# Performance work log

Measured on AMD Instinct MI355X. Metric: run time of the kernel, lower is better.

The kernel has to match this reference:

```python
import jax, jax.numpy as jnp
import numpy as np

N = 100000      # nodes
E = 1600000     # edges
F_IN = 128      # num_node_features
C = 8           # num_classes
EPS = 1e-5


def _lin_init(key, fi, fo):
    k1, k2 = jax.random.split(key)
    s = 1.0 / np.sqrt(fi)
    W = jax.random.uniform(k1, (fi, fo), jnp.float32, -s, s)
    b = jax.random.uniform(k2, (fo,), jnp.float32, -s, s)
    return W, b


def _bn_init(key, f):
    k1, k2, k3, k4 = jax.random.split(key, 4)
    gamma = 1.0 + 0.1 * jax.random.normal(k1, (f,), jnp.float32)
    beta = 0.1 * jax.random.normal(k2, (f,), jnp.float32)
    mean = 0.1 * jax.random.normal(k3, (f,), jnp.float32)
    var = jax.random.uniform(k4, (f,), jnp.float32, 0.5, 1.5)
    return gamma, beta, mean, var


def setup_inputs() -> dict:
    key = jax.random.key(0)
    ks = jax.random.split(key, 10)
    p = {}
    p["x"] = jax.random.normal(ks[0], (N, F_IN), jnp.float32)
    p["edge_index"] = jax.random.randint(ks[1], (2, E), 0, N, jnp.int32)
    p["W1"], p["b1"] = _lin_init(ks[2], F_IN, 64)
    p["g1"], p["be1"], p["m1"], p["v1"] = _bn_init(ks[3], 64)
    p["W2"], p["b2"] = _lin_init(ks[4], 64, 32)
    p["g2"], p["be2"], p["m2"], p["v2"] = _bn_init(ks[5], 32)
    p["W3"], p["b3"] = _lin_init(ks[6], 32, 16)
    p["g3"], p["be3"], p["m3"], p["v3"] = _bn_init(ks[7], 16)
    p["fcW"], p["fcb"] = _lin_init(ks[8], 16, C)
    return p


def _gcn_conv(h, W, b, src, dst, dinv):
    # GCNConv: transform, then symmetric-normalized aggregation with self-loops.
    hw = h @ W                                   # [N, Fout]
    coef = (dinv[src] * dinv[dst])[:, None]      # [E, 1]
    agg = jax.ops.segment_sum(hw[src] * coef, dst, num_segments=N)
    agg = agg + hw * (dinv * dinv)[:, None]      # self-loop contribution
    return agg + b


def _bn(h, g, be, m, v):
    # eval-mode BatchNorm1d with running stats
    return g * (h - m) * jax.lax.rsqrt(v + EPS) + be


def reference(x, edge_index, W1, b1, g1, be1, m1, v1, W2, b2, g2, be2, m2, v2,
              W3, b3, g3, be3, m3, v3, fcW, fcb):
    src, dst = edge_index[0], edge_index[1]
    deg = jax.ops.segment_sum(jnp.ones((E,), jnp.float32), dst, num_segments=N) + 1.0
    dinv = jax.lax.rsqrt(deg)                    # deg >= 1 due to self-loops

    h = jax.nn.relu(_bn(_gcn_conv(x, W1, b1, src, dst, dinv), g1, be1, m1, v1))
    h = jax.nn.relu(_bn(_gcn_conv(h, W2, b2, src, dst, dinv), g2, be2, m2, v2))
    h = jax.nn.relu(_bn(_gcn_conv(h, W3, b3, src, dst, dinv), g3, be3, m3, v3))
    return jax.nn.sigmoid(h @ fcW + fcb)
```

## Files before the change

### kernel.cpp

```cpp
#include <hip/hip_runtime.h>
#include <math.h>

static constexpr int NN = 100000;
static constexpr int NE = 1600000;
static constexpr float BN_EPS = 1e-5f;
static constexpr int K_BKT = (NN + 255) / 256;
static constexpr int CH = 4096;
static constexpr int CAP = 6144;

typedef __attribute__((ext_vector_type(8))) short bf16x8;
typedef __attribute__((ext_vector_type(4))) float f32x4;

__device__ __forceinline__ unsigned short f2bf(float f) {
    unsigned int u = __float_as_uint(f);
    u += 0x7fffu + ((u >> 16) & 1u);
    return (unsigned short)(u >> 16);
}
__device__ __forceinline__ float bf2f(unsigned short b) {
    return __uint_as_float(((unsigned int)b) << 16);
}

__global__ __launch_bounds__(256) void partition_edges(
    const int* __restrict__ src, const int* __restrict__ dst,
    int* __restrict__ bcur, int* __restrict__ staged, int e)
{
    __shared__ int s_out[CH];
    __shared__ int cntL[512];
    __shared__ int gbase[K_BKT];
    __shared__ int curL[K_BKT];

    int tid = threadIdx.x;
    int c0 = blockIdx.x * CH;
    int cend = min(c0 + CH, e);

    for (int i = tid; i < 512; i += 256) cntL[i] = 0;
    __syncthreads();

    for (int i = c0 + tid; i < cend; i += 256)
        atomicAdd(&cntL[((unsigned)dst[i]) >> 8], 1);
    __syncthreads();

    for (int b = tid; b < K_BKT; b += 256) {
        int c = cntL[b];
        gbase[b] = (c > 0) ? (b * CAP + atomicAdd(&bcur[b], c)) : 0;
    }
    __syncthreads();

    for (int d = 1; d < 512; d <<= 1) {
        int x0 = (tid >= d) ? cntL[tid - d] : 0;
        int i1 = tid + 256;
        int x1 = (i1 >= d) ? cntL[i1 - d] : 0;
        __syncthreads();
        cntL[tid] += x0;
        cntL[i1]  += x1;
        __syncthreads();
    }
    for (int b = tid; b < K_BKT; b += 256)
        curL[b] = (b == 0) ? 0 : cntL[b - 1];
    __syncthreads();

    for (int i = c0 + tid; i < cend; i += 256) {
        int s = src[i];
        int d = dst[i];
        int b = ((unsigned)d) >> 8;
        int r = atomicAdd(&curL[b], 1);
        s_out[r] = s | ((d & 255) << 24);
    }
    __syncthreads();

    int wave = tid >> 6, lane = tid & 63;
    for (int b = wave; b < K_BKT; b += 4) {
        int lo = (b == 0) ? 0 : cntL[b - 1];
        int hi = cntL[b];
        int gb = gbase[b];
        for (int i = lo + lane; i < hi; i += 64)
            staged[gb + (i - lo)] = s_out[i];
    }
}

__global__ __launch_bounds__(256) void place_edges(
    const int* __restrict__ bcnt, const int* __restrict__ staged,
    int* __restrict__ esrc, int* __restrict__ off, int* __restrict__ cnt,
    float* __restrict__ dinv, int n)
{
    __shared__ int cntL[256];
    __shared__ int scn[256];
    __shared__ int curL[256];
    int b = blockIdx.x;
    int tid = threadIdx.x;
    int node0 = b << 8;
    int nN = min(256, n - node0);
    int beg = b * CAP;
    int end = beg + bcnt[b];

    cntL[tid] = 0;
    __syncthreads();
    for (int i = beg + tid; i < end; i += 256)
        atomicAdd(&cntL[((unsigned)staged[i]) >> 24], 1);
    __syncthreads();
    scn[tid] = cntL[tid];
    __syncthreads();
    for (int d = 1; d < 256; d <<= 1) {
        int x = (tid >= d) ? scn[tid - d] : 0;
        __syncthreads();
        scn[tid] += x;
        __syncthreads();
    }
    int lofs = (tid == 0) ? 0 : scn[tid - 1];
    if (tid < nN) {
        int node = node0 + tid;
        off[node] = beg + lofs;
        cnt[node] = cntL[tid];
        dinv[node] = rsqrtf((float)cntL[tid] + 1.0f);
    }
    curL[tid] = beg + lofs;
    __syncthreads();
    for (int i = beg + tid; i < end; i += 256) {
        int u = staged[i];
        int pos = atomicAdd(&curL[((unsigned)u) >> 24], 1);
        esrc[pos] = u & 0x00FFFFFF;
    }
}

template<int K, int FOUT>
__device__ __forceinline__ void prep_body(
    const float* __restrict__ W, unsigned short* __restrict__ blob, int t)
{
    constexpr int CT = FOUT / 16;
    int lane = t & 63;
    int ct   = (t >> 6) % CT;
    int ks   = (t >> 6) / CT;
    int col  = ct * 16 + (lane & 15);
    int k0   = ks * 32 + (lane >> 4) * 8;

    union { bf16x8 v; unsigned short e[8]; } u;
#pragma unroll
    for (int j = 0; j < 8; ++j) {
        int kp = k0 + j;
        unsigned short r;
        if (kp < 2 * K) {
            int k = (kp < K) ? kp : kp - K;
            r = f2bf(W[k * FOUT + col]);
        } else {
            float f = W[(kp - 2 * K) * FOUT + col];
            unsigned short h = f2bf(f);
            r = f2bf(f - bf2f(h));
        }
        u.e[j] = r;
    }
    *reinterpret_cast<bf16x8*>(blob + (size_t)t * 8) = u.v;
}

__global__ __launch_bounds__(256) void prep_all(
    const float* __restrict__ W1, const float* __restrict__ W2,
    const float* __restrict__ W3, unsigned short* __restrict__ b1,
    unsigned short* __restrict__ b2, unsigned short* __restrict__ b3,
    int* __restrict__ bcur)
{
    int t = blockIdx.x * 256 + threadIdx.x;
    if (t < 3072)              prep_body<128, 64>(W1, b1, t);
    else if (t < 3840)         prep_body<64, 32>(W2, b2, t - 3072);
    else if (t < 4032)         prep_body<32, 16>(W3, b3, t - 3840);
    else if (t < 4032 + K_BKT) bcur[t - 4032] = 0;
}

template<int K, int FOUT>
__global__ __launch_bounds__(256) void gemm_mfma(
    const float* __restrict__ h, const unsigned short* __restrict__ wtb,
    const float* __restrict__ dinv, unsigned short* __restrict__ hw, int n)
{
    constexpr int PAD = 8;
    constexpr int LDA = 2 * K + PAD;
    constexpr int CT  = FOUT / 16;
    constexpr int KS  = (3 * K) / 32;
    __shared__ unsigned short As[64 * LDA];

    const int tid  = threadIdx.x;
    const int row0 = blockIdx.x * 64;

    constexpr int QK = K / 4;
    for (int i = tid; i < 64 * QK; i += 256) {
        int r = i / QK;
        int q = i % QK;
        int g = row0 + r;
        float4 v;
        if (g < n) v = *reinterpret_cast<const float4*>(h + (size_t)g * K + q * 4);
        else       v = make_float4(0.f, 0.f, 0.f, 0.f);
        ushort4 hi, lo;
        hi.x = f2bf(v.x); lo.x = f2bf(v.x - bf2f(hi.x));
        hi.y = f2bf(v.y); lo.y = f2bf(v.y - bf2f(hi.y));
        hi.z = f2bf(v.z); lo.z = f2bf(v.z - bf2f(hi.z));
        hi.w = f2bf(v.w); lo.w = f2bf(v.w - bf2f(hi.w));
        *reinterpret_cast<ushort4*>(&As[r * LDA + q * 4])     = hi;
        *reinterpret_cast<ushort4*>(&As[r * LDA + K + q * 4]) = lo;
    }
    __syncthreads();

    const int wave = tid >> 6;
    const int lane = tid & 63;
    const int l15  = lane & 15;
    const int kgrp = (lane >> 4) * 8;
    const int arow = wave * 16 + l15;

    const unsigned short* wlane = wtb + lane * 8;

    f32x4 acc[CT];
#pragma unroll
    for (int ct = 0; ct < CT; ++ct) acc[ct] = (f32x4){0.f, 0.f, 0.f, 0.f};

#pragma unroll
    for (int ks = 0; ks < KS; ++ks) {
        int kp = ks * 32 + kgrp;
        int ka = (kp >= 2 * K) ? kp - 2 * K : kp;
        bf16x8 a = *reinterpret_cast<const bf16x8*>(&As[arow * LDA + ka]);
#pragma unroll
        for (int ct = 0; ct < CT; ++ct) {
            bf16x8 b = *reinterpret_cast<const bf16x8*>(wlane + (ks * CT + ct) * 512);
            acc[ct] = __builtin_amdgcn_mfma_f32_16x16x32_bf16(a, b, acc[ct], 0, 0, 0);
        }
    }

    const int rbase = wave * 16 + (lane >> 4) * 4;
    float dv[4];
#pragma unroll
    for (int j = 0; j < 4; ++j) {
        int g = row0 + rbase + j;
        dv[j] = (g < n) ? dinv[g] : 0.f;
    }
#pragma unroll
    for (int ct = 0; ct < CT; ++ct) {
#pragma unroll
        for (int j = 0; j < 4; ++j) {
            int g = row0 + rbase + j;
            if (g < n) hw[(size_t)g * FOUT + ct * 16 + l15] = f2bf(acc[ct][j] * dv[j]);
        }
    }
}

template<int F>
__global__ __launch_bounds__(256) void gather_bn_relu(
    const int* __restrict__ off, const int* __restrict__ cnt,
    const int* __restrict__ esrc, const float* __restrict__ dinv,
    const unsigned short* __restrict__ hw, const float* __restrict__ bias,
    const float* __restrict__ g, const float* __restrict__ be,
    const float* __restrict__ m, const float* __restrict__ v,
    float* __restrict__ hout, int n)
{
    constexpr int SG  = F / 4;
    constexpr int NSG = 64 / SG;
    int node = (blockIdx.x * 256 + threadIdx.x) >> 6;
    if (node >= n) return;
    int lane = threadIdx.x & 63;
    int sg = lane / SG;
    int p  = lane % SG;

    int beg = off[node];
    int num = cnt[node];

    float sx = 0.f, sy = 0.f, sz = 0.f, sw = 0.f;
    int j = sg;
    for (; j + NSG < num; j += 2 * NSG) {
        int s0 = esrc[beg + j];
        int s1 = esrc[beg + j + NSG];
        ushort4 a = *reinterpret_cast<const ushort4*>(hw + (size_t)s0 * F + 4 * p);
        ushort4 b = *reinterpret_cast<const ushort4*>(hw + (size_t)s1 * F + 4 * p);
        sx += bf2f(a.x) + bf2f(b.x);
        sy += bf2f(a.y) + bf2f(b.y);
        sz += bf2f(a.z) + bf2f(b.z);
        sw += bf2f(a.w) + bf2f(b.w);
    }
    if (j < num) {
        int s0 = esrc[beg + j];
        ushort4 a = *reinterpret_cast<const ushort4*>(hw + (size_t)s0 * F + 4 * p);
        sx += bf2f(a.x); sy += bf2f(a.y); sz += bf2f(a.z); sw += bf2f(a.w);
    }
    if (sg == 0) {
        ushort4 a = *reinterpret_cast<const ushort4*>(hw + (size_t)node * F + 4 * p);
        sx += bf2f(a.x); sy += bf2f(a.y); sz += bf2f(a.z); sw += bf2f(a.w);
    }

#pragma unroll
    for (int d = SG; d < 64; d <<= 1) {
        sx += __shfl_xor(sx, d);
        sy += __shfl_xor(sy, d);
        sz += __shfl_xor(sz, d);
        sw += __shfl_xor(sw, d);
    }

    if (sg == 0) {
        int c0 = 4 * p;
        float4 gg = *reinterpret_cast<const float4*>(g + c0);
        float4 vv = *reinterpret_cast<const float4*>(v + c0);
        float4 bb = *reinterpret_cast<const float4*>(bias + c0);
        float4 mm = *reinterpret_cast<const float4*>(m + c0);
        float4 ee = *reinterpret_cast<const float4*>(be + c0);
        float dn = dinv[node];
        float4 y;
        y.x = fmaxf(gg.x * rsqrtf(vv.x + BN_EPS) * (dn * sx + bb.x - mm.x) + ee.x, 0.f);
        y.y = fmaxf(gg.y * rsqrtf(vv.y + BN_EPS) * (dn * sy + bb.y - mm.y) + ee.y, 0.f);
        y.z = fmaxf(gg.z * rsqrtf(vv.z + BN_EPS) * (dn * sz + bb.z - mm.z) + ee.z, 0.f);
        y.w = fmaxf(gg.w * rsqrtf(vv.w + BN_EPS) * (dn * sw + bb.w - mm.w) + ee.w, 0.f);
        *reinterpret_cast<float4*>(hout + (size_t)node * F + c0) = y;
    }
}

__global__ __launch_bounds__(256) void gather_bn_relu_fc(
    const int* __restrict__ off, const int* __restrict__ cnt,
    const int* __restrict__ esrc, const float* __restrict__ dinv,
    const unsigned short* __restrict__ hw, const float* __restrict__ bias,
    const float* __restrict__ g, const float* __restrict__ be,
    const float* __restrict__ m, const float* __restrict__ v,
    const float* __restrict__ fcW, const float* __restrict__ fcb,
    float* __restrict__ out, int n)
{
    constexpr int F = 16, SG = 4, NSG = 16;
    __shared__ float WsF[128];
    __shared__ float bsF[8];
    __shared__ float ybuf[4][16];

    int tid = threadIdx.x;
    if (tid < 128) WsF[tid] = fcW[tid];
    if (tid < 8)   bsF[tid] = fcb[tid];
    __syncthreads();

    int node = (blockIdx.x * 256 + tid) >> 6;
    int wv   = tid >> 6;
    int lane = tid & 63;
    bool act = node < n;

    if (act) {
        int sg = lane / SG;
        int p  = lane % SG;
        int beg = off[node];
        int num = cnt[node];

        float sx = 0.f, sy = 0.f, sz = 0.f, sw = 0.f;
        int j = sg;
        for (; j + NSG < num; j += 2 * NSG) {
            int s0 = esrc[beg + j];
            int s1 = esrc[beg + j + NSG];
            ushort4 a = *reinterpret_cast<const ushort4*>(hw + (size_t)s0 * F + 4 * p);
            ushort4 b = *reinterpret_cast<const ushort4*>(hw + (size_t)s1 * F + 4 * p);
            sx += bf2f(a.x) + bf2f(b.x);
            sy += bf2f(a.y) + bf2f(b.y);
            sz += bf2f(a.z) + bf2f(b.z);
            sw += bf2f(a.w) + bf2f(b.w);
        }
        if (j < num) {
            int s0 = esrc[beg + j];
            ushort4 a = *reinterpret_cast<const ushort4*>(hw + (size_t)s0 * F + 4 * p);
            sx += bf2f(a.x); sy += bf2f(a.y); sz += bf2f(a.z); sw += bf2f(a.w);
        }
        if (sg == 0) {
            ushort4 a = *reinterpret_cast<const ushort4*>(hw + (size_t)node * F + 4 * p);
            sx += bf2f(a.x); sy += bf2f(a.y); sz += bf2f(a.z); sw += bf2f(a.w);
        }

#pragma unroll
        for (int d = SG; d < 64; d <<= 1) {
            sx += __shfl_xor(sx, d);
            sy += __shfl_xor(sy, d);
            sz += __shfl_xor(sz, d);
            sw += __shfl_xor(sw, d);
        }

        if (sg == 0) {
            int c0 = 4 * p;
            float dn = dinv[node];
            ybuf[wv][c0+0] = fmaxf(g[c0+0] * rsqrtf(v[c0+0] + BN_EPS) * (dn * sx + bias[c0+0] - m[c0+0]) + be[c0+0], 0.f);
            ybuf[wv][c0+1] = fmaxf(g[c0+1] * rsqrtf(v[c0+1] + BN_EPS) * (dn * sy + bias[c0+1] - m[c0+1]) + be[c0+1], 0.f);
            ybuf[wv][c0+2] = fmaxf(g[c0+2] * rsqrtf(v[c0+2] + BN_EPS) * (dn * sz + bias[c0+2] - m[c0+2]) + be[c0+2], 0.f);
            ybuf[wv][c0+3] = fmaxf(g[c0+3] * rsqrtf(v[c0+3] + BN_EPS) * (dn * sw + bias[c0+3] - m[c0+3]) + be[c0+3], 0.f);
        }
    }
    __syncthreads();

    if (act && lane < 8) {
        float o = bsF[lane];
#pragma unroll
        for (int k = 0; k < 16; ++k) o += ybuf[wv][k] * WsF[k * 8 + lane];
        out[(size_t)node * 8 + lane] = 1.0f / (1.0f + expf(-o));
    }
}

extern "C" void kernel_launch(void* const* d_in, const int* in_sizes, int n_in,
                              void* d_out, int out_size, void* d_ws, size_t ws_size,
                              hipStream_t stream) {
    const float* x   = (const float*)d_in[0];
    const int*   ei  = (const int*)  d_in[1];
    const float* W1  = (const float*)d_in[2];
    const float* b1  = (const float*)d_in[3];
    const float* g1  = (const float*)d_in[4];
    const float* be1 = (const float*)d_in[5];
    const float* m1  = (const float*)d_in[6];
    const float* v1  = (const float*)d_in[7];
    const float* W2  = (const float*)d_in[8];
    const float* b2  = (const float*)d_in[9];
    const float* g2  = (const float*)d_in[10];
    const float* be2 = (const float*)d_in[11];
    const float* m2  = (const float*)d_in[12];
    const float* v2  = (const float*)d_in[13];
    const float* W3  = (const float*)d_in[14];
    const float* b3  = (const float*)d_in[15];
    const float* g3  = (const float*)d_in[16];
    const float* be3 = (const float*)d_in[17];
    const float* m3  = (const float*)d_in[18];
    const float* v3  = (const float*)d_in[19];
    const float* fcW = (const float*)d_in[20];
    const float* fcb = (const float*)d_in[21];
    float* out = (float*)d_out;

    const int* src = ei;
    const int* dst = ei + NE;

    char* w = (char*)d_ws;
    float* dinv  = (float*)(w + 0);
    int*   cnt   = (int*)  (w + (512 << 10));
    int*   off   = (int*)  (w + (1024 << 10));
    int*   bcur  = (int*)  (w + (1536 << 10));
    int*   staged= (int*)  (w + (2u << 20));
    int*   esrc  = (int*)  (w + (12u << 20));
    unsigned short* wt1 = (unsigned short*)(w + (22u << 20));
    unsigned short* wt2 = wt1 + 24576;
    unsigned short* wt3 = wt2 + 6144;
    unsigned short* hw = (unsigned short*)(w + (24u << 20));
    float* H     = (float*)(w + (40u << 20));

    float* h1 = H;
    float* h2 = H;

    prep_all<<<(4032 + K_BKT + 255) / 256, 256, 0, stream>>>(
        W1, W2, W3, wt1, wt2, wt3, bcur);

    partition_edges<<<(NE + CH - 1) / CH, 256, 0, stream>>>(src, dst, bcur, staged, NE);
    place_edges<<<K_BKT, 256, 0, stream>>>(bcur, staged, esrc, off, cnt, dinv, NN);

    const int GG = (NN * 64 + 255) / 256;

    gemm_mfma<128, 64><<<(NN + 63) / 64, 256, 0, stream>>>(x, wt1, dinv, hw, NN);
    gather_bn_relu<64><<<GG, 256, 0, stream>>>(
        off, cnt, esrc, dinv, hw, b1, g1, be1, m1, v1, h1, NN);

    gemm_mfma<64, 32><<<(NN + 63) / 64, 256, 0, stream>>>(h1, wt2, dinv, hw, NN);
    gather_bn_relu<32><<<GG, 256, 0, stream>>>(
        off, cnt, esrc, dinv, hw, b2, g2, be2, m2, v2, h2, NN);

    gemm_mfma<32, 16><<<(NN + 63) / 64, 256, 0, stream>>>(h2, wt3, dinv, hw, NN);
    gather_bn_relu_fc<<<GG, 256, 0, stream>>>(
        off, cnt, esrc, dinv, hw, b3, g3, be3, m3, v3, fcW, fcb, out, NN);
}
```

Measured before the change: 255.8 us.

## Fuse neighbor gather with next-layer MFMA GEMM and cache edges in registers

After: 244.0 us. 4.6% less time.

```diff
diff --git a/kernel.cpp b/kernel.cpp
--- a/kernel.cpp
+++ b/kernel.cpp
@@ -36,8 +36,16 @@
     for (int i = tid; i < 512; i += 256) cntL[i] = 0;
     __syncthreads();
 
-    for (int i = c0 + tid; i < cend; i += 256)
-        atomicAdd(&cntL[((unsigned)dst[i]) >> 8], 1);
+    int sreg[16], dreg[16];
+#pragma unroll
+    for (int k = 0; k < 16; ++k) {
+        int i = c0 + tid + k * 256;
+        if (i < cend) {
+            sreg[k] = src[i];
+            dreg[k] = dst[i];
+            atomicAdd(&cntL[((unsigned)dreg[k]) >> 8], 1);
+        }
+    }
     __syncthreads();
 
     for (int b = tid; b < K_BKT; b += 256) {
@@ -59,12 +67,14 @@
         curL[b] = (b == 0) ? 0 : cntL[b - 1];
     __syncthreads();
 
-    for (int i = c0 + tid; i < cend; i += 256) {
-        int s = src[i];
-        int d = dst[i];
-        int b = ((unsigned)d) >> 8;
-        int r = atomicAdd(&curL[b], 1);
-        s_out[r] = s | ((d & 255) << 24);
+#pragma unroll
+    for (int k = 0; k < 16; ++k) {
+        int i = c0 + tid + k * 256;
+        if (i < cend) {
+            int b = ((unsigned)dreg[k]) >> 8;
+            int r = atomicAdd(&curL[b], 1);
+            s_out[r] = sreg[k] | ((dreg[k] & 255) << 24);
+        }
     }
     __syncthreads();
 
@@ -123,7 +133,7 @@
 }
 
 template<int K, int FOUT>
-__device__ __forceinline__ void prep_body(
+__device__ __forceinline__ void prep_body3(
     const float* __restrict__ W, unsigned short* __restrict__ blob, int t)
 {
     constexpr int CT = FOUT / 16;
@@ -151,6 +161,34 @@
     *reinterpret_cast<bf16x8*>(blob + (size_t)t * 8) = u.v;
 }
 
+template<int K, int FOUT>
+__device__ __forceinline__ void prep_body2(
+    const float* __restrict__ W, unsigned short* __restrict__ blob, int t)
+{
+    constexpr int CT = FOUT / 16;
+    int lane = t & 63;
+    int ct   = (t >> 6) % CT;
+    int ks   = (t >> 6) / CT;
+    int col  = ct * 16 + (lane & 15);
+    int k0   = ks * 32 + (lane >> 4) * 8;
+
+    union { bf16x8 v; unsigned short e[8]; } u;
+#pragma unroll
+    for (int j = 0; j < 8; ++j) {
+        int kp = k0 + j;
+        unsigned short r;
+        if (kp < K) {
+            r = f2bf(W[kp * FOUT + col]);
+        } else {
+            float f = W[(kp - K) * FOUT + col];
+            unsigned short h = f2bf(f);
+            r = f2bf(f - bf2f(h));
+        }
+        u.e[j] = r;
+    }
+    *reinterpret_cast<bf16x8*>(blob + (size_t)t * 8) = u.v;
+}
+
 __global__ __launch_bounds__(256) void prep_all(
     const float* __restrict__ W1, const float* __restrict__ W2,
     const float* __restrict__ W3, unsigned short* __restrict__ b1,
@@ -158,10 +196,10 @@
     int* __restrict__ bcur)
 {
     int t = blockIdx.x * 256 + threadIdx.x;
-    if (t < 3072)              prep_body<128, 64>(W1, b1, t);
-    else if (t < 3840)         prep_body<64, 32>(W2, b2, t - 3072);
-    else if (t < 4032)         prep_body<32, 16>(W3, b3, t - 3840);
-    else if (t < 4032 + K_BKT) bcur[t - 4032] = 0;
+    if (t < 3072)              prep_body3<128, 64>(W1, b1, t);
+    else if (t < 3584)         prep_body2<64, 32>(W2, b2, t - 3072);
+    else if (t < 3712)         prep_body2<32, 16>(W3, b3, t - 3584);
+    else if (t < 3712 + K_BKT) bcur[t - 3712] = 0;
 }
 
 template<int K, int FOUT>
@@ -237,70 +275,123 @@
     }
 }
 
-template<int F>
-__global__ __launch_bounds__(256) void gather_bn_relu(
+template<int F, int FOUT2>
+__global__ __launch_bounds__(256) void gather_gemm(
     const int* __restrict__ off, const int* __restrict__ cnt,
     const int* __restrict__ esrc, const float* __restrict__ dinv,
-    const unsigned short* __restrict__ hw, const float* __restrict__ bias,
+    const unsigned short* __restrict__ hwin, const float* __restrict__ bias,
     const float* __restrict__ g, const float* __restrict__ be,
     const float* __restrict__ m, const float* __restrict__ v,
-    float* __restrict__ hout, int n)
+    const unsigned short* __restrict__ wtb, unsigned short* __restrict__ hwout,
+    int n)
 {
     constexpr int SG  = F / 4;
     constexpr int NSG = 64 / SG;
-    int node = (blockIdx.x * 256 + threadIdx.x) >> 6;
-    if (node >= n) return;
-    int lane = threadIdx.x & 63;
-    int sg = lane / SG;
-    int p  = lane % SG;
-
-    int beg = off[node];
-    int num = cnt[node];
-
-    float sx = 0.f, sy = 0.f, sz = 0.f, sw = 0.f;
-    int j = sg;
-    for (; j + NSG < num; j += 2 * NSG) {
-        int s0 = esrc[beg + j];
-        int s1 = esrc[beg + j + NSG];
-        ushort4 a = *reinterpret_cast<const ushort4*>(hw + (size_t)s0 * F + 4 * p);
-        ushort4 b = *reinterpret_cast<const ushort4*>(hw + (size_t)s1 * F + 4 * p);
-        sx += bf2f(a.x) + bf2f(b.x);
-        sy += bf2f(a.y) + bf2f(b.y);
-        sz += bf2f(a.z) + bf2f(b.z);
-        sw += bf2f(a.w) + bf2f(b.w);
-    }
-    if (j < num) {
-        int s0 = esrc[beg + j];
-        ushort4 a = *reinterpret_cast<const ushort4*>(hw + (size_t)s0 * F + 4 * p);
-        sx += bf2f(a.x); sy += bf2f(a.y); sz += bf2f(a.z); sw += bf2f(a.w);
-    }
-    if (sg == 0) {
-        ushort4 a = *reinterpret_cast<const ushort4*>(hw + (size_t)node * F + 4 * p);
-        sx += bf2f(a.x); sy += bf2f(a.y); sz += bf2f(a.z); sw += bf2f(a.w);
-    }
-
-#pragma unroll
-    for (int d = SG; d < 64; d <<= 1) {
-        sx += __shfl_xor(sx, d);
-        sy += __shfl_xor(sy, d);
-        sz += __shfl_xor(sz, d);
-        sw += __shfl_xor(sw, d);
-    }
-
-    if (sg == 0) {
-        int c0 = 4 * p;
-        float4 gg = *reinterpret_cast<const float4*>(g + c0);
-        float4 vv = *reinterpret_cast<const float4*>(v + c0);
-        float4 bb = *reinterpret_cast<const float4*>(bias + c0);
-        float4 mm = *reinterpret_cast<const float4*>(m + c0);
-        float4 ee = *reinterpret_cast<const float4*>(be + c0);
-        float dn = dinv[node];
-        float4 y;
-        y.x = fmaxf(gg.x * rsqrtf(vv.x + BN_EPS) * (dn * sx + bb.x - mm.x) + ee.x, 0.f);
-        y.y = fmaxf(gg.y * rsqrtf(vv.y + BN_EPS) * (dn * sy + bb.y - mm.y) + ee.y, 0.f);
-        y.z = fmaxf(gg.z * rsqrtf(vv.z + BN_EPS) * (dn * sz + bb.z - mm.z) + ee.z, 0.f);
-        y.w = fmaxf(gg.w * rsqrtf(vv.w + BN_EPS) * (dn * sw + bb.w - mm.w) + ee.w, 0.f);
-        *reinterpret_cast<float4*>(hout + (size_t)node * F + c0) = y;
+    constexpr int PAD = 8;
+    constexpr int LDA = F + PAD;
+    constexpr int CT  = FOUT2 / 16;
+    constexpr int KS  = (2 * F) / 32;
+    __shared__ unsigned short As[64 * LDA];
+
+    const int tid   = threadIdx.x;
+    const int wv    = tid >> 6;
+    const int lane  = tid & 63;
+    const int node0 = blockIdx.x * 64;
+    const int sg = lane / SG;
+    const int p  = lane % SG;
+
+    for (int t = 0; t < 16; ++t) {
+        int node = node0 + wv * 16 + t;
+        int r = wv * 16 + t;
+        float sx = 0.f, sy = 0.f, sz = 0.f, sw = 0.f;
+        if (node < n) {
+            int beg = off[node];
+            int num = cnt[node];
+            int j = sg;
+            for (; j + NSG < num; j += 2 * NSG) {
+                int s0 = esrc[beg + j];
+                int s1 = esrc[beg + j + NSG];
+                ushort4 a = *reinterpret_cast<const ushort4*>(hwin + (size_t)s0 * F + 4 * p);
+                ushort4 b = *reinterpret_cast<const ushort4*>(hwin + (size_t)s1 * F + 4 * p);
+                sx += bf2f(a.x) + bf2f(b.x);
+                sy += bf2f(a.y) + bf2f(b.y);
+                sz += bf2f(a.z) + bf2f(b.z);
+                sw += bf2f(a.w) + bf2f(b.w);
+            }
+            if (j < num) {
+                int s0 = esrc[beg + j];
+                ushort4 a = *reinterpret_cast<const ushort4*>(hwin + (size_t)s0 * F + 4 * p);
+                sx += bf2f(a.x); sy += bf2f(a.y); sz += bf2f(a.z); sw += bf2f(a.w);
+            }
+            if (sg == 0) {
+                ushort4 a = *reinterpret_cast<const ushort4*>(hwin + (size_t)node * F + 4 * p);
+                sx += bf2f(a.x); sy += bf2f(a.y); sz += bf2f(a.z); sw += bf2f(a.w);
+            }
+        }
+#pragma unroll
+        for (int d = SG; d < 64; d <<= 1) {
+            sx += __shfl_xor(sx, d);
+            sy += __shfl_xor(sy, d);
+            sz += __shfl_xor(sz, d);
+            sw += __shfl_xor(sw, d);
+        }
+        if (sg == 0) {
+            float y0 = 0.f, y1 = 0.f, y2 = 0.f, y3 = 0.f;
+            int c0 = 4 * p;
+            if (node < n) {
+                float dn = dinv[node];
+                float4 gg = *reinterpret_cast<const float4*>(g + c0);
+                float4 vv = *reinterpret_cast<const float4*>(v + c0);
+                float4 bb = *reinterpret_cast<const float4*>(bias + c0);
+                float4 mm = *reinterpret_cast<const float4*>(m + c0);
+                float4 ee = *reinterpret_cast<const float4*>(be + c0);
+                y0 = fmaxf(gg.x * rsqrtf(vv.x + BN_EPS) * (dn * sx + bb.x - mm.x) + ee.x, 0.f);
+                y1 = fmaxf(gg.y * rsqrtf(vv.y + BN_EPS) * (dn * sy + bb.y - mm.y) + ee.y, 0.f);
+                y2 = fmaxf(gg.z * rsqrtf(vv.z + BN_EPS) * (dn * sz + bb.z - mm.z) + ee.z, 0.f);
+                y3 = fmaxf(gg.w * rsqrtf(vv.w + BN_EPS) * (dn * sw + bb.w - mm.w) + ee.w, 0.f);
+            }
+            ushort4 pk;
+            pk.x = f2bf(y0); pk.y = f2bf(y1); pk.z = f2bf(y2); pk.w = f2bf(y3);
+            *reinterpret_cast<ushort4*>(&As[r * LDA + c0]) = pk;
+        }
+    }
+    __syncthreads();
+
+    const int l15  = lane & 15;
+    const int kgrp = (lane >> 4) * 8;
+    const int arow = wv * 16 + l15;
+    const unsigned short* wlane = wtb + lane * 8;
+
+    f32x4 acc[CT];
+#pragma unroll
+    for (int ct = 0; ct < CT; ++ct) acc[ct] = (f32x4){0.f, 0.f, 0.f, 0.f};
+
+#pragma unroll
+    for (int ks = 0; ks < KS; ++ks) {
+        int kp = ks * 32 + kgrp;
+        int ka = (kp >= F) ? kp - F : kp;
+        bf16x8 a = *reinterpret_cast<const bf16x8*>(&As[arow * LDA + ka]);
+#pragma unroll
+        for (int ct = 0; ct < CT; ++ct) {
+            bf16x8 b = *reinterpret_cast<const bf16x8*>(wlane + (ks * CT + ct) * 512);
+            acc[ct] = __builtin_amdgcn_mfma_f32_16x16x32_bf16(a, b, acc[ct], 0, 0, 0);
+        }
+    }
+
+    const int rbase = wv * 16 + (lane >> 4) * 4;
+    float dv[4];
+#pragma unroll
+    for (int j = 0; j < 4; ++j) {
+        int gr = node0 + rbase + j;
+        dv[j] = (gr < n) ? dinv[gr] : 0.f;
+    }
+#pragma unroll
+    for (int ct = 0; ct < CT; ++ct) {
+#pragma unroll
+        for (int j = 0; j < 4; ++j) {
+            int gr = node0 + rbase + j;
+            if (gr < n) hwout[(size_t)gr * FOUT2 + ct * 16 + l15] = f2bf(acc[ct][j] * dv[j]);
+        }
     }
 }
 
@@ -422,30 +513,28 @@
     int*   esrc  = (int*)  (w + (12u << 20));
     unsigned short* wt1 = (unsigned short*)(w + (22u << 20));
     unsigned short* wt2 = wt1 + 24576;
-    unsigned short* wt3 = wt2 + 6144;
-    unsigned short* hw = (unsigned short*)(w + (24u << 20));
-    float* H     = (float*)(w + (40u << 20));
-
-    float* h1 = H;
-    float* h2 = H;
-
-    prep_all<<<(4032 + K_BKT + 255) / 256, 256, 0, stream>>>(
+    unsigned short* wt3 = wt2 + 4096;
+    unsigned short* hw1 = (unsigned short*)(w + (24u << 20));
+    unsigned short* hw2 = (unsigned short*)(w + (38u << 20));
+    unsigned short* hw3 = (unsigned short*)(w + (46u << 20));
+
+    prep_all<<<(3712 + K_BKT + 255) / 256, 256, 0, stream>>>(
         W1, W2, W3, wt1, wt2, wt3, bcur);
 
     partition_edges<<<(NE + CH - 1) / CH, 256, 0, stream>>>(src, dst, bcur, staged, NE);
     place_edges<<<K_BKT, 256, 0, stream>>>(bcur, staged, esrc, off, cnt, dinv, NN);
 
+    const int GB = (NN + 63) / 64;
     const int GG = (NN * 64 + 255) / 256;
 
-    gemm_mfma<128, 64><<<(NN + 63) / 64, 256, 0, stream>>>(x, wt1, dinv, hw, NN);
-    gather_bn_relu<64><<<GG, 256, 0, stream>>>(
-        off, cnt, esrc, dinv, hw, b1, g1, be1, m1, v1, h1, NN);
-
-    gemm_mfma<64, 32><<<(NN + 63) / 64, 256, 0, stream>>>(h1, wt2, dinv, hw, NN);
-    gather_bn_relu<32><<<GG, 256, 0, stream>>>(
-        off, cnt, esrc, dinv, hw, b2, g2, be2, m2, v2, h2, NN);
-
-    gemm_mfma<32, 16><<<(NN + 63) / 64, 256, 0, stream>>>(h2, wt3, dinv, hw, NN);
+    gemm_mfma<128, 64><<<GB, 256, 0, stream>>>(x, wt1, dinv, hw1, NN);
+
+    gather_gemm<64, 32><<<GB, 256, 0, stream>>>(
+        off, cnt, esrc, dinv, hw1, b1, g1, be1, m1, v1, wt2, hw2, NN);
+
+    gather_gemm<32, 16><<<GB, 256, 0, stream>>>(
+        off, cnt, esrc, dinv, hw2, b2, g2, be2, m2, v2, wt3, hw3, NN);
+
     gather_bn_relu_fc<<<GG, 256, 0, stream>>>(
-        off, cnt, esrc, dinv, hw, b3, g3, be3, m3, v3, fcW, fcb, out, NN);
-}
+        off, cnt, esrc, dinv, hw3, b3, g3, be3, m3, v3, fcW, fcb, out, NN);
+}
```
